# Optimization experiments

Measured on AMD Instinct MI355X. Metric: run time of the kernel, lower is better.

## Reference

```python
import jax, jax.numpy as jnp
import numpy as np


def setup_inputs() -> dict:
    key = jax.random.key(0)
    B, H, C, T = 8, 8, 64, 2048
    qkv = jax.random.normal(key, (B, 3 * H * C, T), dtype=jnp.float32)
    return {"qkv": qkv, "n_heads": H}


def reference(qkv, n_heads):
    # qkv: (B, 3*H*C, T)
    bs, width, length = qkv.shape
    ch = width // (3 * n_heads)
    q, k, v = jnp.split(qkv, 3, axis=1)          # each (B, H*C, T)
    scale = ch ** (-0.25)
    q = (q * scale).reshape(bs * n_heads, ch, length)
    k = (k * scale).reshape(bs * n_heads, ch, length)
    v = v.reshape(bs * n_heads, ch, length)
    # weight[b, t, s] = sum_c q[b,c,t] * k[b,c,s]
    weight = jnp.einsum('bct,bcs->bts', q, k)
    weight = jax.nn.softmax(weight.astype(jnp.float32), axis=-1).astype(qkv.dtype)
    out = jnp.einsum('bts,bcs->bct', weight, v)   # (B*H, C, T)
    return out.reshape(bs, n_heads * ch, length)
```

## Files before the change

### kernel.cpp

```cpp
#include <hip/hip_runtime.h>

typedef __bf16 bf16x4 __attribute__((ext_vector_type(4)));
typedef __bf16 bf16x8 __attribute__((ext_vector_type(8)));
typedef float floatx4 __attribute__((ext_vector_type(4)));
typedef float floatx16 __attribute__((ext_vector_type(16)));
typedef unsigned uintx2 __attribute__((ext_vector_type(2)));

#define T_SEQ 2048
#define TTILE 512
#define STILE 64
#define LOG2E_SCALE 0.18033688011112042f

__device__ __forceinline__ unsigned cvt_pk_bf16(float a, float b) {
    unsigned r;
    asm("v_cvt_pk_bf16_f32 %0, %1, %2" : "=v"(r) : "v"(a), "v"(b));
    return r;
}
__device__ __forceinline__ unsigned short bf16_bits(float a) {
    return (unsigned short)((__builtin_bit_cast(unsigned, a) + 0x8000u) >> 16);
}

__global__ __launch_bounds__(512, 2) void attn_fused(
    const float* __restrict__ qkv, float* __restrict__ out)
{
    __shared__ __align__(16) __bf16 Kt[2][STILE][72];
    __shared__ __align__(16) __bf16 Vs[2][64][72];

    const int tid  = threadIdx.x;
    const int lane = tid & 63;
    const int wave = tid >> 6;
    const int l31  = lane & 31;
    const int g    = lane >> 5;

    const int bh = blockIdx.y;
    const int b = bh >> 3, head = bh & 7;
    const size_t in_base = ((size_t)b * 1536 + head * 64) * T_SEQ;
    const float* Qg = qkv + in_base;
    const float* Kg = qkv + in_base + (size_t)512 * T_SEQ;
    const float* Vg = qkv + in_base + (size_t)1024 * T_SEQ;

    const int tcol0 = blockIdx.x * TTILE + wave * 64 + l31;
    const int tcol1 = tcol0 + 32;

    bf16x8 qf[2][4];
    #pragma unroll
    for (int kb = 0; kb < 4; ++kb)
        #pragma unroll
        for (int j = 0; j < 8; ++j) {
            size_t rowoff = (size_t)(kb * 16 + g * 8 + j) * T_SEQ;
            qf[0][kb][j] = (__bf16)(Qg[rowoff + tcol0] * LOG2E_SCALE);
            qf[1][kb][j] = (__bf16)(Qg[rowoff + tcol1] * LOG2E_SCALE);
        }

    floatx16 zf;
    #pragma unroll
    for (int r = 0; r < 16; ++r) zf[r] = 0.0f;

    union U4 { unsigned u[4]; bf16x8 v; };

    floatx16 Oa[2][2];
    Oa[0][0] = zf; Oa[0][1] = zf; Oa[1][0] = zf; Oa[1][1] = zf;
    float dacc0 = 0.0f, dacc1 = 0.0f;

    int cc[2], ss[2];
    size_t goff[2];
    #pragma unroll
    for (int r = 0; r < 2; ++r) {
        int i = tid + r * 512;
        cc[r] = i >> 4;
        ss[r] = (i & 15) * 4;
        goff[r] = (size_t)cc[r] * T_SEQ + ss[r];
    }
    const int ph = (tid >> 1) & 3;

    floatx4 kr[2], vr[2];
    #pragma unroll
    for (int r = 0; r < 2; ++r) {
        kr[r] = *(const floatx4*)(Kg + goff[r]);
        vr[r] = *(const floatx4*)(Vg + goff[r]);
    }
    #pragma unroll
    for (int r = 0; r < 2; ++r) {
        int c = cc[r], s4 = ss[r];
        #pragma unroll
        for (int k = 0; k < 4; ++k) {
            int d = (k + ph) & 3;
            *(unsigned short*)&Kt[0][s4 + d][c] = bf16_bits(kr[r][d]);
        }
        union { unsigned u[2]; bf16x4 v; } vb;
        vb.u[0] = cvt_pk_bf16(vr[r][0], vr[r][1]);
        vb.u[1] = cvt_pk_bf16(vr[r][2], vr[r][3]);
        *(bf16x4*)&Vs[0][c][s4] = vb.v;
    }

#define QKTSTEP(ROWB, SaT0, SaT1)                                             \
    {                                                                         \
        bf16x8 kf = *(const bf16x8*)&KtR[(ROWB) + l31][g * 8];                \
        SaT0 = __builtin_amdgcn_mfma_f32_32x32x16_bf16(kf, qf[0][0], zf, 0, 0, 0); \
        SaT1 = __builtin_amdgcn_mfma_f32_32x32x16_bf16(kf, qf[1][0], zf, 0, 0, 0); \
    }                                                                         \
    _Pragma("unroll")                                                         \
    for (int kb = 1; kb < 4; ++kb) {                                          \
        bf16x8 kf = *(const bf16x8*)&KtR[(ROWB) + l31][kb * 16 + g * 8];      \
        SaT0 = __builtin_amdgcn_mfma_f32_32x32x16_bf16(kf, qf[0][kb], SaT0, 0, 0, 0); \
        SaT1 = __builtin_amdgcn_mfma_f32_32x32x16_bf16(kf, qf[1][kb], SaT1, 0, 0, 0); \
    }

#define SOFTMAX2(SaT0, SaT1, pf)                                              \
    _Pragma("unroll")                                                         \
    for (int tt = 0; tt < 2; ++tt) {                                          \
        const floatx16& Sa_ = tt ? SaT1 : SaT0;                               \
        float p_[16];                                                         \
        _Pragma("unroll")                                                     \
        for (int r = 0; r < 16; ++r)                                          \
            p_[r] = __builtin_amdgcn_exp2f(Sa_[r]);                           \
          \
        {                                                                     \
            float s0_ = (p_[0] + p_[1]) + (p_[2] + p_[3]);                    \
            float s1_ = (p_[4] + p_[5]) + (p_[6] + p_[7]);                    \
            float s2_ = (p_[8] + p_[9]) + (p_[10] + p_[11]);                  \
            float s3_ = (p_[12] + p_[13]) + (p_[14] + p_[15]);                \
            float sA_ = (s0_ + s1_) + (s2_ + s3_);                            \
            if (tt) dacc1 += sA_; else dacc0 += sA_;                          \
        }                                                                     \
        unsigned d_[8];                                                       \
        _Pragma("unroll")                                                     \
        for (int q = 0; q < 8; ++q)                                           \
            d_[q] = cvt_pk_bf16(p_[2 * q], p_[2 * q + 1]);                    \
        _Pragma("unroll")                                                     \
        for (int kb = 0; kb < 2; ++kb) {                                      \
            uintx2 s02 = __builtin_amdgcn_permlane32_swap(                    \
                d_[4 * kb + 0], d_[4 * kb + 2], false, false);                \
            uintx2 s13 = __builtin_amdgcn_permlane32_swap(                    \
                d_[4 * kb + 1], d_[4 * kb + 3], false, false);                \
            U4 fu_;                                                           \
            fu_.u[0] = s02[0]; fu_.u[1] = s13[0];                             \
            fu_.u[2] = s02[1]; fu_.u[3] = s13[1];                             \
            pf[tt][kb] = fu_.v;                                               \
        }                                                                     \
    }

#define PVSTEP(pf, kb2base)                                                   \
    _Pragma("unroll")                                                         \
    for (int mc = 0; mc < 2; ++mc)                                            \
        _Pragma("unroll")                                                     \
        for (int kb = 0; kb < 2; ++kb) {                                      \
            bf16x8 vf = *(const bf16x8*)&VsR[mc * 32 + l31][(kb2base + kb) * 16 + g * 8]; \
            Oa[0][mc] = __builtin_amdgcn_mfma_f32_32x32x16_bf16(vf, pf[0][kb], Oa[0][mc], 0, 0, 0); \
            Oa[1][mc] = __builtin_amdgcn_mfma_f32_32x32x16_bf16(vf, pf[1][kb], Oa[1][mc], 0, 0, 0); \
        }

    for (int it = 0; it < T_SEQ / STILE; ++it) {
        const int rb = it & 1;
        const int s_next = (it + 1) * STILE;
        const bool pref = (s_next < T_SEQ);

        __syncthreads();

        if (pref) {
            #pragma unroll
            for (int r = 0; r < 2; ++r) {
                kr[r] = *(const floatx4*)(Kg + goff[r] + s_next);
                vr[r] = *(const floatx4*)(Vg + goff[r] + s_next);
            }
        }

        const __bf16 (*KtR)[72] = Kt[rb];
        const __bf16 (*VsR)[72] = Vs[rb];

        floatx16 Sa00, Sa01;
        QKTSTEP(0, Sa00, Sa01)
        bf16x8 pfA[2][2];
        SOFTMAX2(Sa00, Sa01, pfA)

        floatx16 Sa10, Sa11;
        QKTSTEP(32, Sa10, Sa11)
        PVSTEP(pfA, 0)

        bf16x8 pfB[2][2];
        SOFTMAX2(Sa10, Sa11, pfB)
        PVSTEP(pfB, 2)

        if (pref) {
            __bf16 (*KtW)[72] = Kt[rb ^ 1];
            __bf16 (*VsW)[72] = Vs[rb ^ 1];
            #pragma unroll
            for (int r = 0; r < 2; ++r) {
                int c = cc[r], s4 = ss[r];
                #pragma unroll
                for (int k = 0; k < 4; ++k) {
                    int d = (k + ph) & 3;
                    *(unsigned short*)&KtW[s4 + d][c] = bf16_bits(kr[r][d]);
                }
                union { unsigned u[2]; bf16x4 v; } vb;
                vb.u[0] = cvt_pk_bf16(vr[r][0], vr[r][1]);
                vb.u[1] = cvt_pk_bf16(vr[r][2], vr[r][3]);
                *(bf16x4*)&VsW[c][s4] = vb.v;
            }
        }
    }

    float rl0 = 1.0f / (dacc0 + __shfl_xor(dacc0, 32));
    float rl1 = 1.0f / (dacc1 + __shfl_xor(dacc1, 32));

    const size_t out_base = ((size_t)b * 512 + head * 64) * T_SEQ;
    #pragma unroll
    for (int mc = 0; mc < 2; ++mc)
        #pragma unroll
        for (int r = 0; r < 16; ++r) {
            int c = mc * 32 + (r & 3) + 8 * (r >> 2) + 4 * g;
            size_t row = out_base + (size_t)c * T_SEQ;
            out[row + tcol0] = Oa[0][mc][r] * rl0;
            out[row + tcol1] = Oa[1][mc][r] * rl1;
        }
}

extern "C" void kernel_launch(void* const* d_in, const int* in_sizes, int n_in,
                              void* d_out, int out_size, void* d_ws, size_t ws_size,
                              hipStream_t stream) {
    const float* qkv = (const float*)d_in[0];
    float* out = (float*)d_out;
    dim3 grid(T_SEQ / TTILE, 64);
    attn_fused<<<grid, dim3(512), 0, stream>>>(qkv, out);
}
```

Measured before the change: 196.4 us.

## Split key sequence in two with workspace partials and a combine kernel

Splits the key/value sequence across two blocks per query tile, doubling the grid from 256 to 512 blocks. Each block writes unnormalized partial outputs and denominators to workspace, and a second kernel sums the partials and normalizes. Blocks are remapped so a head's blocks share an XCD, and launch bounds are raised to 4 blocks per CU. The aim is better CU occupancy on a grid that was too small, paid for with about 64MB of extra workspace traffic and a second launch. The summed partials are valid because the softmax uses no running max.

```diff
diff --git a/kernel.cpp b/kernel.cpp
--- a/kernel.cpp
+++ b/kernel.cpp
@@ -11,6 +11,9 @@
 #define STILE 64
 #define LOG2E_SCALE 0.18033688011112042f
 
+#define WS_O_ELEMS 8388608u
+#define WS_D_ELEMS 131072u
+
 __device__ __forceinline__ unsigned cvt_pk_bf16(float a, float b) {
     unsigned r;
     asm("v_cvt_pk_bf16_f32 %0, %1, %2" : "=v"(r) : "v"(a), "v"(b));
@@ -20,8 +23,9 @@
     return (unsigned short)((__builtin_bit_cast(unsigned, a) + 0x8000u) >> 16);
 }
 
-__global__ __launch_bounds__(512, 2) void attn_fused(
-    const float* __restrict__ qkv, float* __restrict__ out)
+__global__ __launch_bounds__(512, 4) void attn_fused(
+    const float* __restrict__ qkv, float* __restrict__ out,
+    float* __restrict__ wsO, float* __restrict__ wsD)
 {
     __shared__ __align__(16) __bf16 Kt[2][STILE][72];
     __shared__ __align__(16) __bf16 Vs[2][64][72];
@@ -32,14 +36,28 @@
     const int l31  = lane & 31;
     const int g    = lane >> 5;
 
-    const int bh = blockIdx.y;
+    const bool split = (wsO != nullptr);
+    int bh, xb, z, it0, nit;
+    if (split) {
+        const int f   = blockIdx.y * 8 + blockIdx.x;
+        const int xcd = f & 7;
+        const int idx = f >> 3;
+        bh = xcd * 8 + (idx >> 3);
+        const int sub = idx & 7;
+        xb = sub & 3;
+        z  = sub >> 2;
+        it0 = z * 16; nit = 16;
+    } else {
+        bh = blockIdx.y; xb = blockIdx.x; z = 0; it0 = 0; nit = 32;
+    }
+
     const int b = bh >> 3, head = bh & 7;
     const size_t in_base = ((size_t)b * 1536 + head * 64) * T_SEQ;
     const float* Qg = qkv + in_base;
     const float* Kg = qkv + in_base + (size_t)512 * T_SEQ;
     const float* Vg = qkv + in_base + (size_t)1024 * T_SEQ;
 
-    const int tcol0 = blockIdx.x * TTILE + wave * 64 + l31;
+    const int tcol0 = xb * TTILE + wave * 64 + l31;
     const int tcol1 = tcol0 + 32;
 
     bf16x8 qf[2][4];
@@ -69,7 +87,7 @@
         int i = tid + r * 512;
         cc[r] = i >> 4;
         ss[r] = (i & 15) * 4;
-        goff[r] = (size_t)cc[r] * T_SEQ + ss[r];
+        goff[r] = (size_t)cc[r] * T_SEQ + ss[r] + it0 * STILE;
     }
     const int ph = (tid >> 1) & 3;
 
@@ -114,7 +132,6 @@
         _Pragma("unroll")                                                     \
         for (int r = 0; r < 16; ++r)                                          \
             p_[r] = __builtin_amdgcn_exp2f(Sa_[r]);                           \
-          \
         {                                                                     \
             float s0_ = (p_[0] + p_[1]) + (p_[2] + p_[3]);                    \
             float s1_ = (p_[4] + p_[5]) + (p_[6] + p_[7]);                    \
@@ -150,18 +167,18 @@
             Oa[1][mc] = __builtin_amdgcn_mfma_f32_32x32x16_bf16(vf, pf[1][kb], Oa[1][mc], 0, 0, 0); \
         }
 
-    for (int it = 0; it < T_SEQ / STILE; ++it) {
+    for (int it = it0; it < it0 + nit; ++it) {
         const int rb = it & 1;
         const int s_next = (it + 1) * STILE;
-        const bool pref = (s_next < T_SEQ);
+        const bool pref = (it + 1 < it0 + nit);
 
         __syncthreads();
 
         if (pref) {
             #pragma unroll
             for (int r = 0; r < 2; ++r) {
-                kr[r] = *(const floatx4*)(Kg + goff[r] + s_next);
-                vr[r] = *(const floatx4*)(Vg + goff[r] + s_next);
+                kr[r] = *(const floatx4*)(Kg + goff[r] + (s_next - it0 * STILE));
+                vr[r] = *(const floatx4*)(Vg + goff[r] + (s_next - it0 * STILE));
             }
         }
 
@@ -200,19 +217,64 @@
         }
     }
 
-    float rl0 = 1.0f / (dacc0 + __shfl_xor(dacc0, 32));
-    float rl1 = 1.0f / (dacc1 + __shfl_xor(dacc1, 32));
+    float dt0 = dacc0 + __shfl_xor(dacc0, 32);
+    float dt1 = dacc1 + __shfl_xor(dacc1, 32);
 
     const size_t out_base = ((size_t)b * 512 + head * 64) * T_SEQ;
-    #pragma unroll
-    for (int mc = 0; mc < 2; ++mc)
-        #pragma unroll
-        for (int r = 0; r < 16; ++r) {
-            int c = mc * 32 + (r & 3) + 8 * (r >> 2) + 4 * g;
-            size_t row = out_base + (size_t)c * T_SEQ;
-            out[row + tcol0] = Oa[0][mc][r] * rl0;
-            out[row + tcol1] = Oa[1][mc][r] * rl1;
-        }
+    if (split) {
+        float* O = wsO + (size_t)z * WS_O_ELEMS;
+        #pragma unroll
+        for (int mc = 0; mc < 2; ++mc)
+            #pragma unroll
+            for (int r = 0; r < 16; ++r) {
+                int c = mc * 32 + (r & 3) + 8 * (r >> 2) + 4 * g;
+                size_t row = out_base + (size_t)c * T_SEQ;
+                O[row + tcol0] = Oa[0][mc][r];
+                O[row + tcol1] = Oa[1][mc][r];
+            }
+        if (g == 0) {
+            float* D = wsD + (size_t)z * WS_D_ELEMS;
+            D[bh * 2048 + tcol0] = dt0;
+            D[bh * 2048 + tcol1] = dt1;
+        }
+    } else {
+        float rl0 = 1.0f / dt0, rl1 = 1.0f / dt1;
+        #pragma unroll
+        for (int mc = 0; mc < 2; ++mc)
+            #pragma unroll
+            for (int r = 0; r < 16; ++r) {
+                int c = mc * 32 + (r & 3) + 8 * (r >> 2) + 4 * g;
+                size_t row = out_base + (size_t)c * T_SEQ;
+                out[row + tcol0] = Oa[0][mc][r] * rl0;
+                out[row + tcol1] = Oa[1][mc][r] * rl1;
+            }
+    }
+}
+
+__global__ __launch_bounds__(256) void attn_combine(
+    const float* __restrict__ wsO, const float* __restrict__ wsD,
+    float* __restrict__ out)
+{
+    const unsigned N4 = WS_O_ELEMS / 4;
+    const floatx4* O0 = (const floatx4*)wsO;
+    const floatx4* O1 = (const floatx4*)(wsO + WS_O_ELEMS);
+    const floatx4* D0 = (const floatx4*)wsD;
+    const floatx4* D1 = (const floatx4*)(wsD + WS_D_ELEMS);
+    floatx4* outv = (floatx4*)out;
+    for (unsigned i = blockIdx.x * 256 + threadIdx.x; i < N4;
+         i += gridDim.x * 256) {
+        unsigned j = i * 4;
+        unsigned t4   = j & 2047;
+        unsigned hc   = (j >> 11) & 511;
+        unsigned bidx = j >> 20;
+        unsigned bh   = bidx * 8 + (hc >> 6);
+        unsigned di   = (bh * 2048 + t4) >> 2;
+        floatx4 o0 = O0[i], o1 = O1[i], d0 = D0[di], d1 = D1[di];
+        floatx4 r;
+        #pragma unroll
+        for (int k = 0; k < 4; ++k) r[k] = (o0[k] + o1[k]) / (d0[k] + d1[k]);
+        outv[i] = r;
+    }
 }
 
 extern "C" void kernel_launch(void* const* d_in, const int* in_sizes, int n_in,
@@ -220,6 +282,13 @@
                               hipStream_t stream) {
     const float* qkv = (const float*)d_in[0];
     float* out = (float*)d_out;
-    dim3 grid(T_SEQ / TTILE, 64);
-    attn_fused<<<grid, dim3(512), 0, stream>>>(qkv, out);
-}
+    const size_t need = (size_t)(2 * WS_O_ELEMS + 2 * WS_D_ELEMS) * sizeof(float);
+    if (d_ws != nullptr && ws_size >= need) {
+        float* wsO = (float*)d_ws;
+        float* wsD = wsO + 2 * (size_t)WS_O_ELEMS;
+        attn_fused<<<dim3(8, 64), dim3(512), 0, stream>>>(qkv, out, wsO, wsD);
+        attn_combine<<<dim3(2048), dim3(256), 0, stream>>>(wsO, wsD, out);
+    } else {
+        attn_fused<<<dim3(4, 64), dim3(512), 0, stream>>>(qkv, out, nullptr, nullptr);
+    }
+}
```

After: 769.5 us. +291.8%, slower.
